# Kernel optimization log

Measured on AMD Instinct MI355X. Metric: run time of the kernel, lower is better.

## Reference

```python
import jax, jax.numpy as jnp
import numpy as np

C = 64   # in_planes
F = 40   # n_freq
T = 512  # n_frame
B = 16


def setup_inputs() -> dict:
    key = jax.random.key(0)
    kx, kq, kk, kv = jax.random.split(key, 4)
    x = jax.random.normal(kx, (B, C, F, T), dtype=jnp.float32)
    # 1x1 conv weights, no bias: [out_ch, in_ch]
    s = 1.0 / np.sqrt(C)
    Wq = jax.random.uniform(kq, (C, C), dtype=jnp.float32, minval=-s, maxval=s)
    Wk = jax.random.uniform(kk, (C, C), dtype=jnp.float32, minval=-s, maxval=s)
    Wv = jax.random.uniform(kv, (C, C), dtype=jnp.float32, minval=-s, maxval=s)
    return {"x": x, "Wq": Wq, "Wk": Wk, "Wv": Wv}


def _proj_tokens(W, x):
    # 1x1 conv (channel mix) then permute(0,3,2,1) + view -> [B, T, F*C]
    y = jnp.einsum('oc,bcft->btfo', W, x)      # [B, T, F, C]
    b, t, f, c = y.shape
    return y.reshape(b, t, f * c)


def reference(x, Wq, Wk, Wv):
    n_batch, n_planes, n_freq, n_frame = x.shape
    d = n_freq * n_planes
    q = _proj_tokens(Wq, x)                     # [B, T, d]
    k = _proj_tokens(Wk, x)
    v = _proj_tokens(Wv, x)
    scores = jnp.einsum('bqd,bkd->bqk', q, k) / jnp.sqrt(jnp.float32(d))
    attn = jax.nn.softmax(scores, axis=-1)      # [B, T, T]
    out = jnp.einsum('bqk,bkd->bqd', attn, v)   # [B, T, d]
    out = out.reshape(n_batch, n_frame, n_freq, n_planes)
    return jnp.transpose(out, (0, 3, 2, 1))     # [B, C, F, T]
```

## Files before the change

### kernel.cpp

```cpp
#include <hip/hip_runtime.h>

constexpr int B_ = 16, C_ = 64, F_ = 40, T_ = 512;
constexpr int D_ = F_ * C_;
constexpr float SCALE = 0.019764235376052372f;

typedef __attribute__((ext_vector_type(8))) short s16x8;
typedef __attribute__((ext_vector_type(4))) short s16x4;
typedef __attribute__((ext_vector_type(4))) float f32x4;

static __device__ __forceinline__ short f2bf(float f) {
  union { float f; unsigned u; } v; v.f = f;
  unsigned r = v.u + 0x7fffu + ((v.u >> 16) & 1u);
  return (short)(r >> 16);
}

static __device__ __forceinline__ f32x4 mfma16(s16x8 a, s16x8 b, f32x4 c) {
  return __builtin_amdgcn_mfma_f32_16x16x32_bf16(a, b, c, 0, 0, 0);
}

static __device__ __forceinline__ void gl2lds16(const short* g, short* l) {
  __builtin_amdgcn_global_load_lds(
      (const __attribute__((address_space(1))) unsigned int*)g,
      (__attribute__((address_space(3))) unsigned int*)l, 16, 0, 0);
}

__global__ __launch_bounds__(256) void wcvt_kernel(
    const float* __restrict__ Wq, const float* __restrict__ Wk,
    const float* __restrict__ Wv, short* __restrict__ Wb)
{
  const int i = blockIdx.x * 256 + threadIdx.x;
  const float* src = (i < 1024) ? Wq : (i < 2048) ? Wk : Wv;
  const float sc = (i < 1024) ? SCALE : 1.0f;
  const float4 v = *(const float4*)(src + (i & 1023) * 4);
  s16x4 s;
  s[0] = f2bf(v.x * sc); s[1] = f2bf(v.y * sc);
  s[2] = f2bf(v.z * sc); s[3] = f2bf(v.w * sc);
  *(s16x4*)&Wb[i * 4] = s;
}

__global__ __launch_bounds__(256) void proj_kernel(
    const float* __restrict__ x, const short* __restrict__ Wb,
    short* __restrict__ Q, short* __restrict__ K, short* __restrict__ V)
{
  constexpr int XS = 132;
  __shared__ __align__(16) short Xl[64 * XS];

  const int b = blockIdx.z, f = blockIdx.y, tt = blockIdx.x;
  const int tid = threadIdx.x;

  const float* xp = x + (((size_t)b * 64) * 40 + f) * 512 + tt * 128;
  #pragma unroll
  for (int it = 0; it < 8; ++it) {
    const int i = tid + it * 256;
    const int c = i >> 5, j = i & 31;
    const float4 v4 = *(const float4*)(xp + (size_t)c * (F_ * T_) + j * 4);
    s16x4 s4; s4[0] = f2bf(v4.x); s4[1] = f2bf(v4.y);
    s4[2] = f2bf(v4.z); s4[3] = f2bf(v4.w);
    *(s16x4*)&Xl[c * XS + j * 4] = s4;
  }
  __syncthreads();

  const int w = tid >> 6, lane = tid & 63;
  const int quad = lane >> 4, c16 = lane & 15;
  const int tl = w * 32;

  s16x8 bfrag[2][2];
  #pragma unroll
  for (int ni = 0; ni < 2; ++ni)
    #pragma unroll
    for (int ks = 0; ks < 2; ++ks) {
      const int t = tl + ni * 16 + c16;
      const int cb = ks * 32 + quad * 8;
      s16x8 tmp;
      #pragma unroll
      for (int j = 0; j < 8; ++j) tmp[j] = Xl[(cb + j) * XS + t];
      bfrag[ni][ks] = tmp;
    }

  #pragma unroll
  for (int p = 0; p < 3; ++p) {
    const short* Wp = Wb + p * 4096;
    s16x8 wfrag[4][2];
    #pragma unroll
    for (int mi = 0; mi < 4; ++mi)
      #pragma unroll
      for (int ks = 0; ks < 2; ++ks)
        wfrag[mi][ks] = *(const s16x8*)(Wp + (mi * 16 + c16) * 64 + ks * 32 + quad * 8);

    if (p < 2) {
      f32x4 acc[4][2] = {};
      #pragma unroll
      for (int ks = 0; ks < 2; ++ks)
        #pragma unroll
        for (int mi = 0; mi < 4; ++mi)
          #pragma unroll
          for (int ni = 0; ni < 2; ++ni)
            acc[mi][ni] = mfma16(wfrag[mi][ks], bfrag[ni][ks], acc[mi][ni]);
      short* outp = (p == 0) ? Q : K;
      #pragma unroll
      for (int mi = 0; mi < 4; ++mi)
        #pragma unroll
        for (int ni = 0; ni < 2; ++ni) {
          const int t = tt * 128 + tl + ni * 16 + c16;
          const int o = mi * 16 + quad * 4;
          s16x4 s4;
          #pragma unroll
          for (int r = 0; r < 4; ++r) s4[r] = f2bf(acc[mi][ni][r]);
          *(s16x4*)&outp[((size_t)(b * 512 + t)) * D_ + f * 64 + o] = s4;
        }
    } else {
      f32x4 acc[2][4] = {};
      #pragma unroll
      for (int ks = 0; ks < 2; ++ks)
        #pragma unroll
        for (int ni = 0; ni < 2; ++ni)
          #pragma unroll
          for (int mi = 0; mi < 4; ++mi)
            acc[ni][mi] = mfma16(bfrag[ni][ks], wfrag[mi][ks], acc[ni][mi]);
      #pragma unroll
      for (int ni = 0; ni < 2; ++ni)
        #pragma unroll
        for (int mi = 0; mi < 4; ++mi) {
          const int t = tt * 128 + tl + ni * 16 + quad * 4;
          const int o = mi * 16 + c16;
          s16x4 s4;
          #pragma unroll
          for (int r = 0; r < 4; ++r) s4[r] = f2bf(acc[ni][mi][r]);
          *(s16x4*)&V[((size_t)(b * D_ + f * 64 + o)) * 512 + t] = s4;
        }
    }
  }
}

__global__ __launch_bounds__(256) void scores_kernel(
    const short* __restrict__ Q, const short* __restrict__ K,
    float* __restrict__ S)
{
  __shared__ __align__(16) short As[64 * 64];
  __shared__ __align__(16) short Bs[128 * 64];
  const int b = blockIdx.y;
  const int mt = blockIdx.x >> 2, nt = blockIdx.x & 3;
  const int m0 = mt * 64, n0 = nt * 128;
  const int tid = threadIdx.x;
  const int w = tid >> 6, lane = tid & 63, quad = lane >> 4, c16 = lane & 15;
  const int wm = (w >> 1) * 32, wn = (w & 1) * 64;

  const short* qb = Q + (size_t)(b * 512 + m0) * D_;
  const short* kb = K + (size_t)(b * 512 + n0) * D_;

  const short* agp[2];
  short* aldsb[2];
  #pragma unroll
  for (int i = 0; i < 2; ++i) {
    const int s = i * 256 + tid, row = s >> 3;
    const int g = (s & 7) ^ (row & 7);
    agp[i] = qb + (size_t)row * D_ + g * 8;
    aldsb[i] = &As[(i * 256 + w * 64) * 8];
  }
  const short* bgp[4];
  short* bldsb[4];
  #pragma unroll
  for (int i = 0; i < 4; ++i) {
    const int s = i * 256 + tid, row = s >> 3;
    const int g = (s & 7) ^ (row & 7);
    bgp[i] = kb + (size_t)row * D_ + g * 8;
    bldsb[i] = &Bs[(i * 256 + w * 64) * 8];
  }

  const short* amp[2][2];
  #pragma unroll
  for (int mi = 0; mi < 2; ++mi)
    #pragma unroll
    for (int ks = 0; ks < 2; ++ks) {
      const int row = wm + mi * 16 + c16;
      const int g = (ks * 4 + quad) ^ (row & 7);
      amp[mi][ks] = &As[row * 64 + g * 8];
    }
  const short* bmp[4][2];
  #pragma unroll
  for (int ni = 0; ni < 4; ++ni)
    #pragma unroll
    for (int ks = 0; ks < 2; ++ks) {
      const int row = wn + ni * 16 + c16;
      const int g = (ks * 4 + quad) ^ (row & 7);
      bmp[ni][ks] = &Bs[row * 64 + g * 8];
    }

  f32x4 acc[2][4] = {};
  constexpr int NK = D_ / 64;
  for (int kk = 0; kk < NK; ++kk) {
    const int ko = kk * 64;
    __syncthreads();
    #pragma unroll
    for (int i = 0; i < 2; ++i) gl2lds16(agp[i] + ko, aldsb[i]);
    #pragma unroll
    for (int i = 0; i < 4; ++i) gl2lds16(bgp[i] + ko, bldsb[i]);
    __syncthreads();
    s16x8 am[2][2], bm[4][2];
    #pragma unroll
    for (int mi = 0; mi < 2; ++mi)
      #pragma unroll
      for (int ks = 0; ks < 2; ++ks) am[mi][ks] = *(const s16x8*)amp[mi][ks];
    #pragma unroll
    for (int ni = 0; ni < 4; ++ni)
      #pragma unroll
      for (int ks = 0; ks < 2; ++ks) bm[ni][ks] = *(const s16x8*)bmp[ni][ks];
    #pragma unroll
    for (int ks = 0; ks < 2; ++ks)
      #pragma unroll
      for (int mi = 0; mi < 2; ++mi)
        #pragma unroll
        for (int ni = 0; ni < 4; ++ni)
          acc[mi][ni] = mfma16(am[mi][ks], bm[ni][ks], acc[mi][ni]);
  }

  float* sp = S + (size_t)b * 512 * 512;
  #pragma unroll
  for (int mi = 0; mi < 2; ++mi)
    #pragma unroll
    for (int ni = 0; ni < 4; ++ni) {
      const int kcol = n0 + wn + ni * 16 + c16;
      const int qr = m0 + wm + mi * 16 + quad * 4;
      #pragma unroll
      for (int r = 0; r < 4; ++r)
        sp[(size_t)(qr + r) * 512 + kcol] = acc[mi][ni][r];
    }
}

__global__ __launch_bounds__(256) void softmax_kernel(
    const float* __restrict__ S, short* __restrict__ A)
{
  const int b = blockIdx.y;
  const int tid = threadIdx.x, w = tid >> 6, lane = tid & 63;
  const int q = blockIdx.x * 4 + w;
  const float* row = S + ((size_t)b * 512 + q) * 512;

  const float4 v0 = *(const float4*)(row + lane * 4);
  const float4 v1 = *(const float4*)(row + 256 + lane * 4);
  float e[8] = {v0.x, v0.y, v0.z, v0.w, v1.x, v1.y, v1.z, v1.w};

  float m = e[0];
  #pragma unroll
  for (int i = 1; i < 8; ++i) m = fmaxf(m, e[i]);
  #pragma unroll
  for (int off = 1; off < 64; off <<= 1) m = fmaxf(m, __shfl_xor(m, off));

  float s = 0.f;
  #pragma unroll
  for (int i = 0; i < 8; ++i) { e[i] = __expf(e[i] - m); s += e[i]; }
  #pragma unroll
  for (int off = 1; off < 64; off <<= 1) s += __shfl_xor(s, off);

  const float inv = 1.0f / s;
  short* arow = A + ((size_t)b * 512 + q) * 512;
  s16x4 o0, o1;
  #pragma unroll
  for (int i = 0; i < 4; ++i) { o0[i] = f2bf(e[i] * inv); o1[i] = f2bf(e[i + 4] * inv); }
  *(s16x4*)&arow[lane * 4] = o0;
  *(s16x4*)&arow[256 + lane * 4] = o1;
}

__global__ __launch_bounds__(256) void pv_kernel(
    const short* __restrict__ A, const short* __restrict__ V,
    float* __restrict__ out)
{
  __shared__ __align__(16) short As[128 * 64];
  __shared__ __align__(16) short Bs[128 * 64];
  const int b = blockIdx.y;
  const int mt = blockIdx.x / 20, dt = blockIdx.x % 20;
  const int m0 = mt * 128, n0 = dt * 128;
  const int tid = threadIdx.x;
  const int w = tid >> 6, lane = tid & 63, quad = lane >> 4, c16 = lane & 15;
  const int wm = (w >> 1) * 64, wn = (w & 1) * 64;

  const short* ab = A + ((size_t)b * 512 + m0) * 512;
  const short* vb = V + ((size_t)b * D_ + n0) * 512;

  const short* agp[4]; short* aldsb[4];
  const short* bgp[4]; short* bldsb[4];
  #pragma unroll
  for (int i = 0; i < 4; ++i) {
    const int s = i * 256 + tid, row = s >> 3;
    const int g = (s & 7) ^ (row & 7);
    agp[i] = ab + (size_t)row * 512 + g * 8;
    bgp[i] = vb + (size_t)row * 512 + g * 8;
    aldsb[i] = &As[(i * 256 + w * 64) * 8];
    bldsb[i] = &Bs[(i * 256 + w * 64) * 8];
  }

  const short* amp[4][2];
  const short* bmp[4][2];
  #pragma unroll
  for (int mi = 0; mi < 4; ++mi)
    #pragma unroll
    for (int ks = 0; ks < 2; ++ks) {
      const int rowa = wm + mi * 16 + c16;
      const int rowb = wn + mi * 16 + c16;
      amp[mi][ks] = &As[rowa * 64 + (((ks * 4 + quad) ^ (rowa & 7)) * 8)];
      bmp[mi][ks] = &Bs[rowb * 64 + (((ks * 4 + quad) ^ (rowb & 7)) * 8)];
    }

  f32x4 acc[4][4] = {};
  constexpr int NK = 512 / 64;
  for (int kk = 0; kk < NK; ++kk) {
    const int ko = kk * 64;
    __syncthreads();
    #pragma unroll
    for (int i = 0; i < 4; ++i) gl2lds16(agp[i] + ko, aldsb[i]);
    #pragma unroll
    for (int i = 0; i < 4; ++i) gl2lds16(bgp[i] + ko, bldsb[i]);
    __syncthreads();
    s16x8 am[4][2], bm[4][2];
    #pragma unroll
    for (int mi = 0; mi < 4; ++mi)
      #pragma unroll
      for (int ks = 0; ks < 2; ++ks) {
        am[mi][ks] = *(const s16x8*)amp[mi][ks];
        bm[mi][ks] = *(const s16x8*)bmp[mi][ks];
      }
    #pragma unroll
    for (int ks = 0; ks < 2; ++ks)
      #pragma unroll
      for (int mi = 0; mi < 4; ++mi)
        #pragma unroll
        for (int ni = 0; ni < 4; ++ni)
          acc[mi][ni] = mfma16(am[mi][ks], bm[ni][ks], acc[mi][ni]);
  }

  #pragma unroll
  for (int mi = 0; mi < 4; ++mi)
    #pragma unroll
    for (int ni = 0; ni < 4; ++ni) {
      const int d = n0 + wn + ni * 16 + c16;
      const int ff = d >> 6, cc = d & 63;
      const int t = m0 + wm + mi * 16 + quad * 4;
      float4 o4;
      o4.x = acc[mi][ni][0]; o4.y = acc[mi][ni][1];
      o4.z = acc[mi][ni][2]; o4.w = acc[mi][ni][3];
      *(float4*)&out[(((size_t)b * 64 + cc) * 40 + ff) * 512 + t] = o4;
    }
}

extern "C" void kernel_launch(void* const* d_in, const int* in_sizes, int n_in,
                              void* d_out, int out_size, void* d_ws, size_t ws_size,
                              hipStream_t stream)
{
  const float* x  = (const float*)d_in[0];
  const float* Wq = (const float*)d_in[1];
  const float* Wk = (const float*)d_in[2];
  const float* Wv = (const float*)d_in[3];
  float* out = (float*)d_out;

  char* ws = (char*)d_ws;
  constexpr size_t QB = (size_t)B_ * T_ * D_ * 2;
  short* Q  = (short*)(ws);
  short* Kt = (short*)(ws + QB);
  short* Vt = (short*)(ws + 2 * QB);
  float* S  = (float*)(ws + 3 * QB);
  short* Wb = (short*)(ws + 3 * QB);
  short* At = (short*)(ws + 3 * QB + (size_t)B_ * T_ * T_ * 4);

  wcvt_kernel<<<dim3(12), 256, 0, stream>>>(Wq, Wk, Wv, Wb);
  proj_kernel<<<dim3(4, 40, 16), 256, 0, stream>>>(x, Wb, Q, Kt, Vt);
  scores_kernel<<<dim3(32, 16), 256, 0, stream>>>(Q, Kt, S);
  softmax_kernel<<<dim3(128, 16), 256, 0, stream>>>(S, At);
  pv_kernel<<<dim3(80, 16), 256, 0, stream>>>(At, Vt, out);
}
```

Measured before the change: 275.5 us.

## Stage projection outputs through swizzled LDS for coalesced stores; pre-swizzle weight fragments

```diff
diff --git a/kernel.cpp b/kernel.cpp
--- a/kernel.cpp
+++ b/kernel.cpp
@@ -28,22 +28,33 @@
     const float* __restrict__ Wq, const float* __restrict__ Wk,
     const float* __restrict__ Wv, short* __restrict__ Wb)
 {
-  const int i = blockIdx.x * 256 + threadIdx.x;
-  const float* src = (i < 1024) ? Wq : (i < 2048) ? Wk : Wv;
-  const float sc = (i < 1024) ? SCALE : 1.0f;
-  const float4 v = *(const float4*)(src + (i & 1023) * 4);
-  s16x4 s;
-  s[0] = f2bf(v.x * sc); s[1] = f2bf(v.y * sc);
-  s[2] = f2bf(v.z * sc); s[3] = f2bf(v.w * sc);
-  *(s16x4*)&Wb[i * 4] = s;
-}
-
-__global__ __launch_bounds__(256) void proj_kernel(
+  const int n = blockIdx.x * 256 + threadIdx.x;
+  const int p = n >> 9;
+  const int r = n & 511;
+  const int mi = r >> 7;
+  const int ks = (r >> 6) & 1;
+  const int lane = r & 63;
+  const int o = mi * 16 + (lane & 15);
+  const int cb = ks * 32 + (lane >> 4) * 8;
+  const float* src = (p == 0) ? Wq : (p == 1) ? Wk : Wv;
+  const float sc = (p == 0) ? SCALE : 1.0f;
+  const float4 a = *(const float4*)(src + o * 64 + cb);
+  const float4 b2 = *(const float4*)(src + o * 64 + cb + 4);
+  s16x8 s;
+  s[0] = f2bf(a.x * sc);  s[1] = f2bf(a.y * sc);
+  s[2] = f2bf(a.z * sc);  s[3] = f2bf(a.w * sc);
+  s[4] = f2bf(b2.x * sc); s[5] = f2bf(b2.y * sc);
+  s[6] = f2bf(b2.z * sc); s[7] = f2bf(b2.w * sc);
+  *(s16x8*)&Wb[n * 8] = s;
+}
+
+__global__ __launch_bounds__(256, 2) void proj_kernel(
     const float* __restrict__ x, const short* __restrict__ Wb,
     short* __restrict__ Q, short* __restrict__ K, short* __restrict__ V)
 {
   constexpr int XS = 132;
   __shared__ __align__(16) short Xl[64 * XS];
+  char* Ost = (char*)Xl;
 
   const int b = blockIdx.z, f = blockIdx.y, tt = blockIdx.x;
   const int tid = threadIdx.x;
@@ -76,16 +87,16 @@
       for (int j = 0; j < 8; ++j) tmp[j] = Xl[(cb + j) * XS + t];
       bfrag[ni][ks] = tmp;
     }
+  __syncthreads();
 
   #pragma unroll
   for (int p = 0; p < 3; ++p) {
-    const short* Wp = Wb + p * 4096;
     s16x8 wfrag[4][2];
     #pragma unroll
     for (int mi = 0; mi < 4; ++mi)
       #pragma unroll
       for (int ks = 0; ks < 2; ++ks)
-        wfrag[mi][ks] = *(const s16x8*)(Wp + (mi * 16 + c16) * 64 + ks * 32 + quad * 8);
+        wfrag[mi][ks] = *(const s16x8*)(Wb + ((p * 8 + mi * 2 + ks) * 64 + lane) * 8);
 
     if (p < 2) {
       f32x4 acc[4][2] = {};
@@ -96,18 +107,30 @@
           #pragma unroll
           for (int ni = 0; ni < 2; ++ni)
             acc[mi][ni] = mfma16(wfrag[mi][ks], bfrag[ni][ks], acc[mi][ni]);
-      short* outp = (p == 0) ? Q : K;
+      __syncthreads();
       #pragma unroll
       for (int mi = 0; mi < 4; ++mi)
         #pragma unroll
         for (int ni = 0; ni < 2; ++ni) {
-          const int t = tt * 128 + tl + ni * 16 + c16;
-          const int o = mi * 16 + quad * 4;
+          const int trow = tl + ni * 16 + c16;
+          unsigned addr = trow * 128 + (mi * 32 + quad * 8);
+          addr ^= (unsigned)((trow & 7) << 4);
           s16x4 s4;
           #pragma unroll
           for (int r = 0; r < 4; ++r) s4[r] = f2bf(acc[mi][ni][r]);
-          *(s16x4*)&outp[((size_t)(b * 512 + t)) * D_ + f * 64 + o] = s4;
+          *(s16x4*)(Ost + addr) = s4;
         }
+      __syncthreads();
+      short* outp = (p == 0) ? Q : K;
+      #pragma unroll
+      for (int pass = 0; pass < 4; ++pass) {
+        const int row = pass * 32 + (tid >> 3);
+        const int s16off = tid & 7;
+        unsigned a2 = row * 128 + s16off * 16;
+        a2 ^= (unsigned)((row & 7) << 4);
+        const s16x8 vz = *(const s16x8*)(Ost + a2);
+        *(s16x8*)&outp[(size_t)(b * 512 + tt * 128 + row) * D_ + f * 64 + s16off * 8] = vz;
+      }
     } else {
       f32x4 acc[2][4] = {};
       #pragma unroll
@@ -117,18 +140,31 @@
           #pragma unroll
           for (int mi = 0; mi < 4; ++mi)
             acc[ni][mi] = mfma16(bfrag[ni][ks], wfrag[mi][ks], acc[ni][mi]);
+      __syncthreads();
       #pragma unroll
       for (int ni = 0; ni < 2; ++ni)
         #pragma unroll
         for (int mi = 0; mi < 4; ++mi) {
-          const int t = tt * 128 + tl + ni * 16 + quad * 4;
-          const int o = mi * 16 + c16;
+          const int orow = mi * 16 + c16;
+          unsigned addr = orow * 256 + (tl + ni * 16 + quad * 4) * 2;
+          addr ^= (unsigned)((orow & 7) << 4);
           s16x4 s4;
           #pragma unroll
           for (int r = 0; r < 4; ++r) s4[r] = f2bf(acc[ni][mi][r]);
-          *(s16x4*)&V[((size_t)(b * D_ + f * 64 + o)) * 512 + t] = s4;
+          *(s16x4*)(Ost + addr) = s4;
         }
-    }
+      __syncthreads();
+      #pragma unroll
+      for (int pass = 0; pass < 4; ++pass) {
+        const int row = pass * 16 + (tid >> 4);
+        const int s16off = tid & 15;
+        unsigned a2 = row * 256 + s16off * 16;
+        a2 ^= (unsigned)((row & 7) << 4);
+        const s16x8 vz = *(const s16x8*)(Ost + a2);
+        *(s16x8*)&V[((size_t)(b * D_ + f * 64 + row)) * 512 + tt * 128 + s16off * 8] = vz;
+      }
+    }
+    if (p < 2) __syncthreads();
   }
 }
 
@@ -360,7 +396,7 @@
   short* Wb = (short*)(ws + 3 * QB);
   short* At = (short*)(ws + 3 * QB + (size_t)B_ * T_ * T_ * 4);
 
-  wcvt_kernel<<<dim3(12), 256, 0, stream>>>(Wq, Wk, Wv, Wb);
+  wcvt_kernel<<<dim3(6), 256, 0, stream>>>(Wq, Wk, Wv, Wb);
   proj_kernel<<<dim3(4, 40, 16), 256, 0, stream>>>(x, Wb, Q, Kt, Vt);
   scores_kernel<<<dim3(32, 16), 256, 0, stream>>>(Q, Kt, S);
   softmax_kernel<<<dim3(128, 16), 256, 0, stream>>>(S, At);
```

Result: faster. 251.4 us (-8.8%).
